# Optimization experiments

Hardware: AMD Instinct MI355X
Metric: run time of the kernel (lower is better)

The kernel has to match this reference:

```python
import jax, jax.numpy as jnp
import numpy as np

N_NODES = 50000
N_EDGES = 1_250_000
D_FEAT = 64


def setup_inputs() -> dict:
    key = jax.random.key(0)
    k1, k2, k3 = jax.random.split(key, 3)
    graph_embedding = jax.random.normal(k1, (N_NODES, D_FEAT), dtype=jnp.float32)
    src = jax.random.randint(k2, (N_EDGES,), 0, N_NODES, dtype=jnp.int64)
    dst = jax.random.randint(k3, (N_EDGES,), 0, N_NODES, dtype=jnp.int64)
    return {"graph_embedding": graph_embedding, "src": src, "dst": dst}


def reference(graph_embedding, src, dst):
    # DGL update_all(copy_u('ft','m'), sum('m','ft')):
    # out[v] = sum over edges (u->v) of graph_embedding[u]
    messages = graph_embedding[src]  # [E, d] gather
    out = jax.ops.segment_sum(messages, dst, num_segments=graph_embedding.shape[0])
    return out
```

## Files before the change

kernel.cpp:

```cpp
#include <hip/hip_runtime.h>


#define D_FEAT 64
#define BSHIFT 7
#define BNODES 128
#define MAXNB  512
#define CAP4   6144
#define CHUNK  8192
#define CAP1   96

static __device__ __forceinline__ unsigned short f2bf(float f) {
    unsigned u = __float_as_uint(f);
    u += 0x7fffu + ((u >> 16) & 1u);
    return (unsigned short)(u >> 16);
}

__global__ __launch_bounds__(256) void cvt_bf16_kernel(
    const float4* __restrict__ in, uint2* __restrict__ outp, int n4)
{
    int i = blockIdx.x * blockDim.x + threadIdx.x;
    if (i >= n4) return;
    float4 x = in[i];
    uint2 o;
    o.x = (unsigned)f2bf(x.x) | ((unsigned)f2bf(x.y) << 16);
    o.y = (unsigned)f2bf(x.z) | ((unsigned)f2bf(x.w) << 16);
    outp[i] = o;
}

__global__ __launch_bounds__(512) void partition_kernel(
    const int* __restrict__ src,
    const int* __restrict__ dst,
    unsigned*  __restrict__ cursor,
    unsigned*  __restrict__ packed,
    int n_edges, int nb)
{
    __shared__ unsigned lhist[MAXNB];
    __shared__ unsigned lbase[MAXNB];
    int t = threadIdx.x;
    int base = blockIdx.x * CHUNK;
    int cnt = n_edges - base; if (cnt > CHUNK) cnt = CHUNK; if (cnt < 0) cnt = 0;
    int nv = cnt >> 2;
    const int4* d4 = (const int4*)(dst + base);
    const int4* s4 = (const int4*)(src + base);

    for (int i = t; i < nb; i += 512) lhist[i] = 0;
    __syncthreads();

    for (int i = t; i < nv; i += 512) {
        int4 d = d4[i];
        atomicAdd(&lhist[d.x >> BSHIFT], 1u);
        atomicAdd(&lhist[d.y >> BSHIFT], 1u);
        atomicAdd(&lhist[d.z >> BSHIFT], 1u);
        atomicAdd(&lhist[d.w >> BSHIFT], 1u);
    }
    for (int i = nv * 4 + t; i < cnt; i += 512)
        atomicAdd(&lhist[dst[base + i] >> BSHIFT], 1u);
    __syncthreads();

    for (int i = t; i < nb; i += 512) {
        unsigned c = lhist[i];
        lbase[i] = c ? atomicAdd(&cursor[i], c) : 0u;
        lhist[i] = 0;
    }
    __syncthreads();

    for (int i = t; i < nv; i += 512) {
        int4 d = d4[i];
        int4 s = s4[i];
        #pragma unroll
        for (int k = 0; k < 4; ++k) {
            int dd = (k == 0) ? d.x : (k == 1) ? d.y : (k == 2) ? d.z : d.w;
            int ss = (k == 0) ? s.x : (k == 1) ? s.y : (k == 2) ? s.z : s.w;
            int b = dd >> BSHIFT;
            unsigned off = atomicAdd(&lhist[b], 1u);
            unsigned pos = lbase[b] + off;
            if (pos < CAP4)
                packed[(size_t)b * CAP4 + pos] =
                    (unsigned)ss | ((unsigned)(dd & (BNODES - 1)) << 16);
        }
    }
    for (int i = nv * 4 + t; i < cnt; i += 512) {
        int dd = dst[base + i];
        int b = dd >> BSHIFT;
        unsigned off = atomicAdd(&lhist[b], 1u);
        unsigned pos = lbase[b] + off;
        if (pos < CAP4)
            packed[(size_t)b * CAP4 + pos] =
                (unsigned)src[base + i] | ((unsigned)(dd & (BNODES - 1)) << 16);
    }
}

__global__ __launch_bounds__(512) void sort_kernel(
    const unsigned* __restrict__ cursor,
    const unsigned* __restrict__ packed,
    unsigned short* __restrict__ sorted,
    unsigned*       __restrict__ startcnt,
    int n_nodes)
{
    __shared__ unsigned lpk[CAP4];
    __shared__ unsigned hist[BNODES];
    __shared__ unsigned cur[BNODES];
    int b = blockIdx.x;
    int t = threadIdx.x;
    int node_base = b << BSHIFT;
    int nn = n_nodes - node_base; if (nn > BNODES) nn = BNODES;

    int cnt = (int)cursor[b]; if (cnt > CAP4) cnt = CAP4;
    const unsigned* pk = packed + (size_t)b * CAP4;

    if (t < BNODES) hist[t] = 0;
    __syncthreads();

    for (int i = t; i < cnt; i += 512) {
        unsigned p = pk[i];
        lpk[i] = p;
        atomicAdd(&hist[p >> 16], 1u);
    }
    __syncthreads();

    if (t < 64) {
        int l = t;
        unsigned v0 = hist[2 * l], v1 = hist[2 * l + 1];
        unsigned s = v0 + v1;
        unsigned inc = s;
        #pragma unroll
        for (int d = 1; d < 64; d <<= 1) {
            unsigned u = __shfl_up(inc, d);
            if (l >= d) inc += u;
        }
        unsigned exc = inc - s;
        cur[2 * l]     = exc;
        cur[2 * l + 1] = exc + v0;
        if (2 * l < nn)     startcnt[node_base + 2 * l]     = (exc << 16) | v0;
        if (2 * l + 1 < nn) startcnt[node_base + 2 * l + 1] = ((exc + v0) << 16) | v1;
    }
    __syncthreads();

    unsigned short* so = sorted + (size_t)b * CAP4;
    for (int i = t; i < cnt; i += 512) {
        unsigned p = lpk[i];
        unsigned pos = atomicAdd(&cur[p >> 16], 1u);
        so[pos] = (unsigned short)(p & 0xffffu);
    }
}

__global__ __launch_bounds__(256) void gather_kernel(
    const unsigned short* __restrict__ embh,
    const unsigned short* __restrict__ sorted,
    const unsigned*       __restrict__ startcnt,
    float*                __restrict__ out,
    int n_nodes)
{
    int v    = blockIdx.x * 4 + (threadIdx.x >> 6);
    int lane = threadIdx.x & 63;
    if (v >= n_nodes) return;
    int rgrp = lane >> 3;
    int c8   = lane & 7;

    unsigned sc = startcnt[v];
    int cnt = (int)(sc & 0xffffu);
    const unsigned short* list =
        sorted + ((size_t)(v >> BSHIFT)) * CAP4 + (sc >> 16);

    float a0=0.f,a1=0.f,a2=0.f,a3=0.f,a4=0.f,a5=0.f,a6=0.f,a7=0.f;

    for (int base = 0; base < cnt; base += 64) {
        int m = cnt - base; if (m > 64) m = 64;
        unsigned sv = (lane < m) ? (unsigned)list[base + lane] : 0u;
        #pragma unroll 2
        for (int j = 0; j < m; j += 8) {
            int r = j + rgrp;
            unsigned s = (unsigned)__shfl((int)sv, r);
            if (r < m) {
                uint4 h = *(const uint4*)(embh + ((size_t)s << 6) + c8 * 8);
                a0 += __uint_as_float((h.x & 0xffffu) << 16);
                a1 += __uint_as_float(h.x & 0xffff0000u);
                a2 += __uint_as_float((h.y & 0xffffu) << 16);
                a3 += __uint_as_float(h.y & 0xffff0000u);
                a4 += __uint_as_float((h.z & 0xffffu) << 16);
                a5 += __uint_as_float(h.z & 0xffff0000u);
                a6 += __uint_as_float((h.w & 0xffffu) << 16);
                a7 += __uint_as_float(h.w & 0xffff0000u);
            }
        }
    }
    #define RED8(mask) \
        a0 += __shfl_xor(a0, mask); a1 += __shfl_xor(a1, mask); \
        a2 += __shfl_xor(a2, mask); a3 += __shfl_xor(a3, mask); \
        a4 += __shfl_xor(a4, mask); a5 += __shfl_xor(a5, mask); \
        a6 += __shfl_xor(a6, mask); a7 += __shfl_xor(a7, mask);
    RED8(8); RED8(16); RED8(32);
    #undef RED8

    if (lane < 8) {
        float4* o4 = (float4*)(out + (size_t)v * D_FEAT + lane * 8);
        o4[0] = make_float4(a0, a1, a2, a3);
        o4[1] = make_float4(a4, a5, a6, a7);
    }
}

__global__ __launch_bounds__(256) void count_scatter_kernel(
    const int* __restrict__ src, const int* __restrict__ dst,
    int* __restrict__ cnt, int* __restrict__ bucket, int n_edges)
{
    int e = blockIdx.x * blockDim.x + threadIdx.x;
    if (e >= n_edges) return;
    int s = src[e], d = dst[e];
    int pos = atomicAdd(&cnt[d], 1);
    if (pos < CAP1) bucket[(size_t)d * CAP1 + pos] = s;
}

__global__ __launch_bounds__(256) void gather_sum_kernel(
    const float* __restrict__ emb, const int* __restrict__ cnt,
    const int* __restrict__ bucket, float* __restrict__ out, int n_nodes)
{
    int v = (blockIdx.x * blockDim.x + threadIdx.x) >> 6;
    int lane = threadIdx.x & 63;
    if (v >= n_nodes) return;
    int n = cnt[v]; if (n > CAP1) n = CAP1;
    const int* b = bucket + (size_t)v * CAP1;
    float acc = 0.f;
    for (int j = 0; j < n; ++j)
        acc += emb[(size_t)b[j] * D_FEAT + lane];
    out[(size_t)v * D_FEAT + lane] = acc;
}

__global__ __launch_bounds__(256) void scatter_sum_fallback(
    const float* __restrict__ emb, const int* __restrict__ src,
    const int* __restrict__ dst, float* __restrict__ out, int n_edges)
{
    int gid = blockIdx.x * blockDim.x + threadIdx.x;
    int e = gid >> 4;
    if (e >= n_edges) return;
    int c = gid & 15;
    int s = src[e], d = dst[e];
    const float4* emb4 = (const float4*)emb;
    float4 v = emb4[(size_t)s * 16 + c];
    float* o = out + (size_t)d * D_FEAT + c * 4;
    atomicAdd(o + 0, v.x); atomicAdd(o + 1, v.y);
    atomicAdd(o + 2, v.z); atomicAdd(o + 3, v.w);
}

extern "C" void kernel_launch(void* const* d_in, const int* in_sizes, int n_in,
                              void* d_out, int out_size, void* d_ws, size_t ws_size,
                              hipStream_t stream) {
    const float* emb = (const float*)d_in[0];
    const int*   src = (const int*)d_in[1];
    const int*   dst = (const int*)d_in[2];
    float*       out = (float*)d_out;

    int n_edges = in_sizes[1];
    int n_nodes = out_size / D_FEAT;
    int nb = (n_nodes + BNODES - 1) >> BSHIFT;

    size_t cur_b  = 4096;
    size_t pack_b = (size_t)nb * CAP4 * sizeof(unsigned);
    size_t sort_b = (size_t)nb * CAP4 * sizeof(unsigned short);
    size_t sc_b   = ((size_t)n_nodes * sizeof(unsigned) + 255) & ~255ull;
    size_t embh_b = (size_t)n_nodes * D_FEAT * sizeof(unsigned short);

    if (n_nodes <= 65536 && nb <= MAXNB &&
        ws_size >= cur_b + pack_b + sort_b + sc_b + embh_b) {
        char* p = (char*)d_ws;
        unsigned*       cursor   = (unsigned*)p;       p += cur_b;
        unsigned*       packed   = (unsigned*)p;       p += pack_b;
        unsigned short* sorted   = (unsigned short*)p; p += sort_b;
        unsigned*       startcnt = (unsigned*)p;       p += sc_b;
        unsigned short* embh     = (unsigned short*)p;

        hipMemsetAsync(cursor, 0, (size_t)nb * sizeof(unsigned), stream);

        int n4 = n_nodes * D_FEAT / 4;
        cvt_bf16_kernel<<<(n4 + 255) / 256, 256, 0, stream>>>(
            (const float4*)emb, (uint2*)embh, n4);

        partition_kernel<<<(n_edges + CHUNK - 1) / CHUNK, 512, 0, stream>>>(
            src, dst, cursor, packed, n_edges, nb);

        sort_kernel<<<nb, 512, 0, stream>>>(
            cursor, packed, sorted, startcnt, n_nodes);

        gather_kernel<<<(n_nodes + 3) / 4, 256, 0, stream>>>(
            embh, sorted, startcnt, out, n_nodes);
    } else if (ws_size >= (size_t)n_nodes * sizeof(int) * (1 + CAP1)) {
        int* cnt    = (int*)d_ws;
        int* bucket = (int*)((char*)d_ws + (size_t)n_nodes * sizeof(int));
        hipMemsetAsync(cnt, 0, (size_t)n_nodes * sizeof(int), stream);
        count_scatter_kernel<<<(n_edges + 255) / 256, 256, 0, stream>>>(
            src, dst, cnt, bucket, n_edges);
        gather_sum_kernel<<<(n_nodes * 64 + 255) / 256, 256, 0, stream>>>(
            emb, cnt, bucket, out, n_nodes);
    } else {
        hipMemsetAsync(d_out, 0, (size_t)out_size * sizeof(float), stream);
        long long total = (long long)n_edges * 16;
        scatter_sum_fallback<<<(int)((total + 255) / 256), 256, 0, stream>>>(
            emb, src, dst, out, n_edges);
    }
}
```

Baseline: 125.1 us.

## Fuse bf16 conversion with partition and sort with gather, halve bucket size

Merges the bf16 conversion and edge partitioning into one launch, with the blocks split by role. The partition step now stages the packed edges in shared memory in a single global read instead of reading dst twice. The per-bucket sort and the gather are fused into one kernel that keeps the sorted source list in LDS, which removes the global sorted and startcnt arrays and two kernel launches. Buckets shrink to 64 nodes (capacity 2048) so each block handles fewer edges. This risks lower parallelism in the gather, since each wave walks 16 nodes serially, and tighter capacity clipping if degrees are skewed.

```diff
diff --git a/kernel.cpp b/kernel.cpp
--- a/kernel.cpp
+++ b/kernel.cpp
@@ -2,11 +2,11 @@
 
 
 #define D_FEAT 64
-#define BSHIFT 7
-#define BNODES 128
-#define MAXNB  512
-#define CAP4   6144
-#define CHUNK  8192
+#define BSHIFT 6
+#define BNODES 64
+#define MAXNB  1024
+#define CAP2   2048
+#define PCHUNK 4096
 #define CAP1   96
 
 static __device__ __forceinline__ unsigned short f2bf(float f) {
@@ -15,103 +15,107 @@
     return (unsigned short)(u >> 16);
 }
 
-__global__ __launch_bounds__(256) void cvt_bf16_kernel(
-    const float4* __restrict__ in, uint2* __restrict__ outp, int n4)
-{
-    int i = blockIdx.x * blockDim.x + threadIdx.x;
-    if (i >= n4) return;
-    float4 x = in[i];
-    uint2 o;
-    o.x = (unsigned)f2bf(x.x) | ((unsigned)f2bf(x.y) << 16);
-    o.y = (unsigned)f2bf(x.z) | ((unsigned)f2bf(x.w) << 16);
-    outp[i] = o;
-}
-
-__global__ __launch_bounds__(512) void partition_kernel(
-    const int* __restrict__ src,
-    const int* __restrict__ dst,
-    unsigned*  __restrict__ cursor,
-    unsigned*  __restrict__ packed,
-    int n_edges, int nb)
-{
+__global__ __launch_bounds__(256) void fused_cvt_partition_kernel(
+    const float4* __restrict__ emb4,
+    uint2*        __restrict__ embh2,
+    const int*    __restrict__ src,
+    const int*    __restrict__ dst,
+    unsigned*     __restrict__ cursor,
+    unsigned*     __restrict__ packed,
+    int n4, int cvt_blocks, int n_edges, int nb)
+{
+    __shared__ unsigned lpk[PCHUNK];
     __shared__ unsigned lhist[MAXNB];
     __shared__ unsigned lbase[MAXNB];
-    int t = threadIdx.x;
-    int base = blockIdx.x * CHUNK;
-    int cnt = n_edges - base; if (cnt > CHUNK) cnt = CHUNK; if (cnt < 0) cnt = 0;
+
+    if ((int)blockIdx.x < cvt_blocks) {
+        int i = blockIdx.x * 256 + threadIdx.x;
+        if (i < n4) {
+            float4 x = emb4[i];
+            uint2 o;
+            o.x = (unsigned)f2bf(x.x) | ((unsigned)f2bf(x.y) << 16);
+            o.y = (unsigned)f2bf(x.z) | ((unsigned)f2bf(x.w) << 16);
+            embh2[i] = o;
+        }
+        return;
+    }
+
+    int pb   = blockIdx.x - cvt_blocks;
+    int t    = threadIdx.x;
+    int base = pb * PCHUNK;
+    int cnt  = n_edges - base; if (cnt > PCHUNK) cnt = PCHUNK; if (cnt < 0) cnt = 0;
+
+    for (int i = t; i < nb; i += 256) lhist[i] = 0;
+    __syncthreads();
+
     int nv = cnt >> 2;
     const int4* d4 = (const int4*)(dst + base);
     const int4* s4 = (const int4*)(src + base);
-
-    for (int i = t; i < nb; i += 512) lhist[i] = 0;
-    __syncthreads();
-
-    for (int i = t; i < nv; i += 512) {
+    for (int i = t; i < nv; i += 256) {
         int4 d = d4[i];
-        atomicAdd(&lhist[d.x >> BSHIFT], 1u);
-        atomicAdd(&lhist[d.y >> BSHIFT], 1u);
-        atomicAdd(&lhist[d.z >> BSHIFT], 1u);
-        atomicAdd(&lhist[d.w >> BSHIFT], 1u);
-    }
-    for (int i = nv * 4 + t; i < cnt; i += 512)
-        atomicAdd(&lhist[dst[base + i] >> BSHIFT], 1u);
-    __syncthreads();
-
-    for (int i = t; i < nb; i += 512) {
+        int4 s = s4[i];
+        uint4 pkw;
+        pkw.x = ((unsigned)(d.x >> BSHIFT) << 22) | ((unsigned)(d.x & (BNODES-1)) << 16) | (unsigned)s.x;
+        pkw.y = ((unsigned)(d.y >> BSHIFT) << 22) | ((unsigned)(d.y & (BNODES-1)) << 16) | (unsigned)s.y;
+        pkw.z = ((unsigned)(d.z >> BSHIFT) << 22) | ((unsigned)(d.z & (BNODES-1)) << 16) | (unsigned)s.z;
+        pkw.w = ((unsigned)(d.w >> BSHIFT) << 22) | ((unsigned)(d.w & (BNODES-1)) << 16) | (unsigned)s.w;
+        ((uint4*)lpk)[i] = pkw;
+        atomicAdd(&lhist[pkw.x >> 22], 1u);
+        atomicAdd(&lhist[pkw.y >> 22], 1u);
+        atomicAdd(&lhist[pkw.z >> 22], 1u);
+        atomicAdd(&lhist[pkw.w >> 22], 1u);
+    }
+    for (int i = nv * 4 + t; i < cnt; i += 256) {
+        int dd = dst[base + i];
+        unsigned p = ((unsigned)(dd >> BSHIFT) << 22) |
+                     ((unsigned)(dd & (BNODES-1)) << 16) | (unsigned)src[base + i];
+        lpk[i] = p;
+        atomicAdd(&lhist[p >> 22], 1u);
+    }
+    __syncthreads();
+
+    for (int i = t; i < nb; i += 256) {
         unsigned c = lhist[i];
         lbase[i] = c ? atomicAdd(&cursor[i], c) : 0u;
         lhist[i] = 0;
     }
     __syncthreads();
 
-    for (int i = t; i < nv; i += 512) {
-        int4 d = d4[i];
-        int4 s = s4[i];
-        #pragma unroll
-        for (int k = 0; k < 4; ++k) {
-            int dd = (k == 0) ? d.x : (k == 1) ? d.y : (k == 2) ? d.z : d.w;
-            int ss = (k == 0) ? s.x : (k == 1) ? s.y : (k == 2) ? s.z : s.w;
-            int b = dd >> BSHIFT;
-            unsigned off = atomicAdd(&lhist[b], 1u);
-            unsigned pos = lbase[b] + off;
-            if (pos < CAP4)
-                packed[(size_t)b * CAP4 + pos] =
-                    (unsigned)ss | ((unsigned)(dd & (BNODES - 1)) << 16);
-        }
-    }
-    for (int i = nv * 4 + t; i < cnt; i += 512) {
-        int dd = dst[base + i];
-        int b = dd >> BSHIFT;
+    for (int i = t; i < cnt; i += 256) {
+        unsigned p = lpk[i];
+        unsigned b = p >> 22;
         unsigned off = atomicAdd(&lhist[b], 1u);
         unsigned pos = lbase[b] + off;
-        if (pos < CAP4)
-            packed[(size_t)b * CAP4 + pos] =
-                (unsigned)src[base + i] | ((unsigned)(dd & (BNODES - 1)) << 16);
-    }
-}
-
-__global__ __launch_bounds__(512) void sort_kernel(
-    const unsigned* __restrict__ cursor,
-    const unsigned* __restrict__ packed,
-    unsigned short* __restrict__ sorted,
-    unsigned*       __restrict__ startcnt,
+        if (pos < CAP2)
+            packed[(size_t)b * CAP2 + pos] = p & 0x3fffffu;
+    }
+}
+
+__global__ __launch_bounds__(256) void sortgather_kernel(
+    const unsigned short* __restrict__ embh,
+    const unsigned*       __restrict__ cursor,
+    const unsigned*       __restrict__ packed,
+    float*                __restrict__ out,
     int n_nodes)
 {
-    __shared__ unsigned lpk[CAP4];
-    __shared__ unsigned hist[BNODES];
-    __shared__ unsigned cur[BNODES];
+    __shared__ unsigned       lpk[CAP2];
+    __shared__ unsigned short slist[CAP2];
+    __shared__ unsigned       hist[BNODES];
+    __shared__ unsigned       cur[BNODES];
+    __shared__ unsigned       stc[BNODES];
+
     int b = blockIdx.x;
     int t = threadIdx.x;
     int node_base = b << BSHIFT;
     int nn = n_nodes - node_base; if (nn > BNODES) nn = BNODES;
 
-    int cnt = (int)cursor[b]; if (cnt > CAP4) cnt = CAP4;
-    const unsigned* pk = packed + (size_t)b * CAP4;
+    int cnt = (int)cursor[b]; if (cnt > CAP2) cnt = CAP2;
+    const unsigned* pk = packed + (size_t)b * CAP2;
 
     if (t < BNODES) hist[t] = 0;
     __syncthreads();
 
-    for (int i = t; i < cnt; i += 512) {
+    for (int i = t; i < cnt; i += 256) {
         unsigned p = pk[i];
         lpk[i] = p;
         atomicAdd(&hist[p >> 16], 1u);
@@ -119,59 +123,43 @@
     __syncthreads();
 
     if (t < 64) {
-        int l = t;
-        unsigned v0 = hist[2 * l], v1 = hist[2 * l + 1];
-        unsigned s = v0 + v1;
-        unsigned inc = s;
+        unsigned v = hist[t];
+        unsigned inc = v;
         #pragma unroll
         for (int d = 1; d < 64; d <<= 1) {
             unsigned u = __shfl_up(inc, d);
-            if (l >= d) inc += u;
-        }
-        unsigned exc = inc - s;
-        cur[2 * l]     = exc;
-        cur[2 * l + 1] = exc + v0;
-        if (2 * l < nn)     startcnt[node_base + 2 * l]     = (exc << 16) | v0;
-        if (2 * l + 1 < nn) startcnt[node_base + 2 * l + 1] = ((exc + v0) << 16) | v1;
-    }
-    __syncthreads();
-
-    unsigned short* so = sorted + (size_t)b * CAP4;
-    for (int i = t; i < cnt; i += 512) {
+            if (t >= d) inc += u;
+        }
+        unsigned exc = inc - v;
+        cur[t] = exc;
+        stc[t] = (exc << 16) | v;
+    }
+    __syncthreads();
+
+    for (int i = t; i < cnt; i += 256) {
         unsigned p = lpk[i];
         unsigned pos = atomicAdd(&cur[p >> 16], 1u);
-        so[pos] = (unsigned short)(p & 0xffffu);
-    }
-}
-
-__global__ __launch_bounds__(256) void gather_kernel(
-    const unsigned short* __restrict__ embh,
-    const unsigned short* __restrict__ sorted,
-    const unsigned*       __restrict__ startcnt,
-    float*                __restrict__ out,
-    int n_nodes)
-{
-    int v    = blockIdx.x * 4 + (threadIdx.x >> 6);
-    int lane = threadIdx.x & 63;
-    if (v >= n_nodes) return;
+        slist[pos] = (unsigned short)(p & 0xffffu);
+    }
+    __syncthreads();
+
+    int w    = t >> 6;
+    int lane = t & 63;
     int rgrp = lane >> 3;
     int c8   = lane & 7;
 
-    unsigned sc = startcnt[v];
-    int cnt = (int)(sc & 0xffffu);
-    const unsigned short* list =
-        sorted + ((size_t)(v >> BSHIFT)) * CAP4 + (sc >> 16);
-
-    float a0=0.f,a1=0.f,a2=0.f,a3=0.f,a4=0.f,a5=0.f,a6=0.f,a7=0.f;
-
-    for (int base = 0; base < cnt; base += 64) {
-        int m = cnt - base; if (m > 64) m = 64;
-        unsigned sv = (lane < m) ? (unsigned)list[base + lane] : 0u;
-        #pragma unroll 2
-        for (int j = 0; j < m; j += 8) {
+    for (int ni = 0; ni < 16; ++ni) {
+        int dl = w * 16 + ni;
+        if (dl >= nn) break;
+        unsigned sc = stc[dl];
+        int st = (int)(sc >> 16);
+        int cn = (int)(sc & 0xffffu);
+
+        float a0=0.f,a1=0.f,a2=0.f,a3=0.f,a4=0.f,a5=0.f,a6=0.f,a7=0.f;
+        for (int j = 0; j < cn; j += 8) {
             int r = j + rgrp;
-            unsigned s = (unsigned)__shfl((int)sv, r);
-            if (r < m) {
+            if (r < cn) {
+                unsigned s = (unsigned)slist[st + r];
                 uint4 h = *(const uint4*)(embh + ((size_t)s << 6) + c8 * 8);
                 a0 += __uint_as_float((h.x & 0xffffu) << 16);
                 a1 += __uint_as_float(h.x & 0xffff0000u);
@@ -183,19 +171,19 @@
                 a7 += __uint_as_float(h.w & 0xffff0000u);
             }
         }
-    }
-    #define RED8(mask) \
-        a0 += __shfl_xor(a0, mask); a1 += __shfl_xor(a1, mask); \
-        a2 += __shfl_xor(a2, mask); a3 += __shfl_xor(a3, mask); \
-        a4 += __shfl_xor(a4, mask); a5 += __shfl_xor(a5, mask); \
-        a6 += __shfl_xor(a6, mask); a7 += __shfl_xor(a7, mask);
-    RED8(8); RED8(16); RED8(32);
-    #undef RED8
-
-    if (lane < 8) {
-        float4* o4 = (float4*)(out + (size_t)v * D_FEAT + lane * 8);
-        o4[0] = make_float4(a0, a1, a2, a3);
-        o4[1] = make_float4(a4, a5, a6, a7);
+        #define RED8(mask) \
+            a0 += __shfl_xor(a0, mask); a1 += __shfl_xor(a1, mask); \
+            a2 += __shfl_xor(a2, mask); a3 += __shfl_xor(a3, mask); \
+            a4 += __shfl_xor(a4, mask); a5 += __shfl_xor(a5, mask); \
+            a6 += __shfl_xor(a6, mask); a7 += __shfl_xor(a7, mask);
+        RED8(8); RED8(16); RED8(32);
+        #undef RED8
+
+        if (lane < 8) {
+            float4* o4 = (float4*)(out + (size_t)(node_base + dl) * D_FEAT + lane * 8);
+            o4[0] = make_float4(a0, a1, a2, a3);
+            o4[1] = make_float4(a4, a5, a6, a7);
+        }
     }
 }
 
@@ -253,35 +241,28 @@
     int n_nodes = out_size / D_FEAT;
     int nb = (n_nodes + BNODES - 1) >> BSHIFT;
 
-    size_t cur_b  = 4096;
-    size_t pack_b = (size_t)nb * CAP4 * sizeof(unsigned);
-    size_t sort_b = (size_t)nb * CAP4 * sizeof(unsigned short);
-    size_t sc_b   = ((size_t)n_nodes * sizeof(unsigned) + 255) & ~255ull;
+    size_t cur_b  = 8192;
+    size_t pack_b = (size_t)nb * CAP2 * sizeof(unsigned);
     size_t embh_b = (size_t)n_nodes * D_FEAT * sizeof(unsigned short);
 
     if (n_nodes <= 65536 && nb <= MAXNB &&
-        ws_size >= cur_b + pack_b + sort_b + sc_b + embh_b) {
+        ws_size >= cur_b + pack_b + embh_b) {
         char* p = (char*)d_ws;
-        unsigned*       cursor   = (unsigned*)p;       p += cur_b;
-        unsigned*       packed   = (unsigned*)p;       p += pack_b;
-        unsigned short* sorted   = (unsigned short*)p; p += sort_b;
-        unsigned*       startcnt = (unsigned*)p;       p += sc_b;
-        unsigned short* embh     = (unsigned short*)p;
+        unsigned*       cursor = (unsigned*)p;        p += cur_b;
+        unsigned*       packed = (unsigned*)p;        p += pack_b;
+        unsigned short* embh   = (unsigned short*)p;
 
         hipMemsetAsync(cursor, 0, (size_t)nb * sizeof(unsigned), stream);
 
         int n4 = n_nodes * D_FEAT / 4;
-        cvt_bf16_kernel<<<(n4 + 255) / 256, 256, 0, stream>>>(
-            (const float4*)emb, (uint2*)embh, n4);
-
-        partition_kernel<<<(n_edges + CHUNK - 1) / CHUNK, 512, 0, stream>>>(
-            src, dst, cursor, packed, n_edges, nb);
-
-        sort_kernel<<<nb, 512, 0, stream>>>(
-            cursor, packed, sorted, startcnt, n_nodes);
-
-        gather_kernel<<<(n_nodes + 3) / 4, 256, 0, stream>>>(
-            embh, sorted, startcnt, out, n_nodes);
+        int cvt_blocks = (n4 + 255) / 256;
+        int p_blocks   = (n_edges + PCHUNK - 1) / PCHUNK;
+        fused_cvt_partition_kernel<<<cvt_blocks + p_blocks, 256, 0, stream>>>(
+            (const float4*)emb, (uint2*)embh, src, dst, cursor, packed,
+            n4, cvt_blocks, n_edges, nb);
+
+        sortgather_kernel<<<nb, 256, 0, stream>>>(
+            embh, cursor, packed, out, n_nodes);
     } else if (ws_size >= (size_t)n_nodes * sizeof(int) * (1 + CAP1)) {
         int* cnt    = (int*)d_ws;
         int* bucket = (int*)((char*)d_ws + (size_t)n_nodes * sizeof(int));
```

After: 136.5 us. 9.2% more time.
